# Optimization experiments

Measured on AMD Instinct MI355X. Metric: run time of the kernel, lower is better.

Reference implementation:

```python
import jax, jax.numpy as jnp
import numpy as np
import math

B_SZ, T, D_IN, D_OUT, N = 8, 4096, 1024, 1024, 512
RMIN, RMAX, MAX_PHASE = 0.9, 1.0, 6.283


def setup_inputs() -> dict:
    key = jax.random.key(0)
    ks = jax.random.split(key, 9)
    x = jax.random.normal(ks[0], (B_SZ, T, D_IN), dtype=jnp.float32)
    u1 = jax.random.uniform(ks[1], (N,), dtype=jnp.float32)
    u2 = jax.random.uniform(ks[2], (N,), dtype=jnp.float32)
    nu_log = jnp.log(-0.5 * jnp.log(u1 * (RMAX + RMIN) * (RMAX - RMIN) + RMIN ** 2))
    theta_log = jnp.log(MAX_PHASE * u2)
    lam_mod = jnp.exp(-jnp.exp(nu_log))
    gamma_log = jnp.log(jnp.sqrt(1.0 - jnp.square(lam_mod)))
    B_re = jax.random.normal(ks[3], (N, D_IN), dtype=jnp.float32) / math.sqrt(2 * D_IN)
    B_im = jax.random.normal(ks[4], (N, D_IN), dtype=jnp.float32) / math.sqrt(2 * D_IN)
    C_re = jax.random.normal(ks[5], (D_OUT, N), dtype=jnp.float32) / math.sqrt(N)
    C_im = jax.random.normal(ks[6], (D_OUT, N), dtype=jnp.float32) / math.sqrt(N)
    D = jax.random.normal(ks[7], (D_OUT, D_IN), dtype=jnp.float32) / math.sqrt(D_IN)
    return {"x": x, "nu_log": nu_log, "theta_log": theta_log, "gamma_log": gamma_log,
            "B_re": B_re, "B_im": B_im, "C_re": C_re, "C_im": C_im, "D": D}


def reference(x, nu_log, theta_log, gamma_log, B_re, B_im, C_re, C_im, D):
    # Diagonal complex transition Lambda = exp(-exp(nu_log)) * exp(i*exp(theta_log))
    lam = jnp.exp(-jnp.exp(nu_log) + 1j * jnp.exp(theta_log))  # [N] complex64
    gamma = jnp.exp(gamma_log)  # [N]
    Bmat = B_re + 1j * B_im  # [N, D_IN]
    # Input projection for all timesteps at once: b_t = gamma * (B @ u_t)
    Bu = jnp.einsum('bti,ni->btn', x.astype(Bmat.dtype), Bmat) * gamma  # [B,T,N] complex
    # Parallel (associative) scan of x_t = lam * x_{t-1} + b_t over the time axis
    A = jnp.broadcast_to(lam, Bu.shape)

    def combine(e1, e2):
        a1, b1 = e1
        a2, b2 = e2
        return a1 * a2, a2 * b1 + b2

    _, states = jax.lax.associative_scan(combine, (A, Bu), axis=1)  # states: [B,T,N] complex
    Cmat = C_re + 1j * C_im  # [D_OUT, N]
    y = jnp.einsum('btn,on->bto', states, Cmat).real + jnp.einsum('bti,oi->bto', x, D)
    return y
```

## Files before the change

### kernel.cpp

```cpp
#include <hip/hip_runtime.h>
#include <stdint.h>


#define BSZ   8
#define TLEN  4096
#define DIN   1024
#define DOUT  1024
#define NST   512
#define M_TOT (BSZ * TLEN)
#define NC    32
#define CL    128

#define WOFF  8192
#define NBUF  16384

#define PLA   4096
#define OBUFS 12288

typedef __attribute__((ext_vector_type(8))) short bf16x8;
typedef __attribute__((ext_vector_type(4))) float f32x4;

__device__ __forceinline__ float s2f(short s) {
  unsigned v = ((unsigned)(unsigned short)s) << 16;
  return __builtin_bit_cast(float, v);
}
__device__ __forceinline__ short f2s_rne(float f) {
  unsigned u = __builtin_bit_cast(unsigned, f);
  unsigned r = (u + 0x7FFFu + ((u >> 16) & 1u)) >> 16;
  return (short)r;
}
__device__ __forceinline__ void round8(const float4 v0, const float4 v1, bf16x8& hv) {
  const float f[8] = {v0.x, v0.y, v0.z, v0.w, v1.x, v1.y, v1.z, v1.w};
  #pragma unroll
  for (int j = 0; j < 8; ++j) hv[j] = f2s_rne(f[j]);
}

__device__ __forceinline__ void gload16(const short* g, short* l) {
  __builtin_amdgcn_global_load_lds(
      (const __attribute__((address_space(1))) void*)g,
      (__attribute__((address_space(3))) void*)l, 16, 0, 0);
}


__device__ __forceinline__ void stage_one256(
    const short* __restrict__ Ag, const short* __restrict__ Wg,
    const int lda, const int ldb, const int m0, const int n0, const int k0,
    short* lbuf, const int ch, const int lane)
{
  const int q  = (lane & 3) ^ ((lane >> 3) & 3);
  const int gr = lane >> 2;
  const short* g;
  int r0, ld, dst;
  if (ch < 16) { g = Ag; r0 = m0 + ch * 16;        ld = lda; dst = ch * 512; }
  else         { g = Wg; r0 = n0 + (ch - 16) * 16; ld = ldb; dst = WOFF + (ch - 16) * 512; }
  gload16(g + (size_t)(r0 + gr) * ld + k0 + q * 8, lbuf + dst);
}

template<int NT>
__device__ __forceinline__ void gemm256(
    const short* __restrict__ Ap, const short* __restrict__ Wp,
    const int lda, const int ldb, const int m0, const int n0, const int tid,
    f32x4 (&acc)[8][4], short* lds)
{
  const int lane = tid & 63, w = tid >> 6, wm = w >> 2, wn = w & 3;
  const int lr = lane & 15, kg = lane >> 4;
  const int qo = (kg ^ ((lr >> 1) & 3)) * 8;

  #pragma unroll
  for (int j = 0; j < 4; ++j)
    stage_one256(Ap, Wp, lda, ldb, m0, n0, 0, lds, w * 4 + j, lane);
  #pragma unroll
  for (int j = 0; j < 4; ++j)
    stage_one256(Ap, Wp, lda, ldb, m0, n0, 32, lds + NBUF, w * 4 + j, lane);

  int c0 = 0;
  for (int k = 0; k < NT; ++k) {
    short* cur = lds + c0 * NBUF;
    int cs = c0 + 2; if (cs >= 3) cs -= 3;
    short* nx2 = lds + cs * NBUF;

    if (k + 1 < NT) asm volatile("s_waitcnt vmcnt(4)" ::: "memory");
    else            asm volatile("s_waitcnt vmcnt(0)" ::: "memory");
    __builtin_amdgcn_s_barrier();

    bf16x8 wv[4];
    #pragma unroll
    for (int ph = 0; ph < 4; ++ph) {
      if (ph == 0) {
        #pragma unroll
        for (int nf = 0; nf < 4; ++nf)
          wv[nf] = *(const bf16x8*)&cur[WOFF + (wn * 64 + nf * 16 + lr) * 32 + qo];
      }
      const int mi0 = ph * 2;
      const bf16x8 a0 = *(const bf16x8*)&cur[(wm * 128 + mi0 * 16 + lr) * 32 + qo];
      const bf16x8 a1 = *(const bf16x8*)&cur[(wm * 128 + (mi0 + 1) * 16 + lr) * 32 + qo];
      if (k + 2 < NT)
        stage_one256(Ap, Wp, lda, ldb, m0, n0, (k + 2) * 32, nx2, w * 4 + ph, lane);
      __builtin_amdgcn_s_barrier();
      asm volatile("s_waitcnt lgkmcnt(0)" ::: "memory");
      __builtin_amdgcn_sched_barrier(0);
      __builtin_amdgcn_s_setprio(1);
      #pragma unroll
      for (int nf = 0; nf < 4; ++nf) {
        acc[mi0][nf]     = __builtin_amdgcn_mfma_f32_16x16x32_bf16(a0, wv[nf], acc[mi0][nf], 0, 0, 0);
        acc[mi0 + 1][nf] = __builtin_amdgcn_mfma_f32_16x16x32_bf16(a1, wv[nf], acc[mi0 + 1][nf], 0, 0, 0);
      }
      __builtin_amdgcn_s_setprio(0);
      __builtin_amdgcn_s_barrier();
    }
    c0 = (c0 == 2) ? 0 : c0 + 1;
  }
}

__device__ __forceinline__ void map256(const int bid, int& mb, int& nb) {
  const int xcd = bid & 7;
  const int j   = bid >> 3;
  mb = xcd * 16 + (j >> 2);
  nb = j & 3;
}

__device__ __forceinline__ void stage_cx(
    const short* __restrict__ Ag, const short* __restrict__ Wg,
    const int lda, const int ldb, const int m0, const int n0, const int k0,
    short* lbuf, const int w, const int lane)
{
  const int q  = (lane & 3) ^ ((lane >> 3) & 3);
  const int gr = lane >> 2;
  #pragma unroll
  for (int j = 0; j < 3; ++j) {
    const int ch = w * 3 + j;
    const short* g;
    int r0, ld, dst;
    if (ch < 8) { g = Ag; r0 = m0 + ch * 16;        ld = lda; dst = ch * 512; }
    else        { g = Wg; r0 = n0 + (ch - 8) * 16;  ld = ldb; dst = PLA + (ch - 8) * 512; }
    gload16(g + (size_t)(r0 + gr) * ld + k0 + q * 8, lbuf + dst);
  }
}

__device__ __forceinline__ void gemm_fb(
    const float* __restrict__ Af, const short* __restrict__ Wp,
    const int lda, const int ldb, const int K, const int m0, const int n0, const int tid,
    f32x4 (&acc)[4][4], short* lds)
{
  const int lane = tid & 63, w = tid >> 6, wm = w >> 2, wn = w & 3;
  const int r = tid & 127, e = (tid >> 7) & 3;
  float4 pa[2];
  {
    const float* p = Af + (size_t)(m0 + r) * lda + e * 8;
    pa[0] = *(const float4*)(p);
    pa[1] = *(const float4*)(p + 4);
  }
  for (int k0 = 0; k0 < K; k0 += 32) {
    __syncthreads();
    {
      bf16x8 hv;
      round8(pa[0], pa[1], hv);
      const int f = (r >> 1) & 3;
      *(bf16x8*)&lds[r * 32 + ((e ^ f) * 8)] = hv;
    }
    {
      const int q = (lane & 3) ^ ((lane >> 3) & 3);
      const int gr = lane >> 2;
      #pragma unroll
      for (int i = 0; i < 2; ++i)
        gload16(Wp + (size_t)(n0 + (2 * w + i) * 16 + gr) * ldb + k0 + q * 8,
                lds + PLA + (2 * w + i) * 512);
    }
    __syncthreads();
    if (k0 + 32 < K) {
      const float* p = Af + (size_t)(m0 + r) * lda + (k0 + 32) + e * 8;
      pa[0] = *(const float4*)(p);
      pa[1] = *(const float4*)(p + 4);
    }
    const int lr = lane & 15, kg = lane >> 4;
    const int qo = (kg ^ ((lr >> 1) & 3)) * 8;
    bf16x8 aw[4], bw[4];
    #pragma unroll
    for (int mi = 0; mi < 4; ++mi)
      aw[mi] = *(const bf16x8*)&lds[(wm * 64 + mi * 16 + lr) * 32 + qo];
    #pragma unroll
    for (int ni = 0; ni < 4; ++ni)
      bw[ni] = *(const bf16x8*)&lds[PLA + (wn * 64 + ni * 16 + lr) * 32 + qo];
    #pragma unroll
    for (int ni = 0; ni < 4; ++ni)
      #pragma unroll
      for (int mi = 0; mi < 4; ++mi)
        acc[mi][ni] = __builtin_amdgcn_mfma_f32_16x16x32_bf16(aw[mi], bw[ni], acc[mi][ni], 0, 0, 0);
  }
  __syncthreads();
}

template<int NT>
__device__ __forceinline__ void gemm_pl(
    const short* __restrict__ Ap, const short* __restrict__ Wp,
    const int lda, const int ldb, const int m0, const int n0, const int tid,
    f32x4 (&acc)[4][4], short* lds)
{
  const int lane = tid & 63, w = tid >> 6, wm = w >> 2, wn = w & 3;
  const int lr = lane & 15, kg = lane >> 4;
  const int qo = (kg ^ ((lr >> 1) & 3)) * 8;
  stage_cx(Ap, Wp, lda, ldb, m0, n0, 0, lds, w, lane);
  for (int k = 0; k < NT; ++k) {
    short* cur = lds + (k & 1) * OBUFS;
    if (k + 1 < NT) {
      stage_cx(Ap, Wp, lda, ldb, m0, n0, (k + 1) * 32, lds + ((k + 1) & 1) * OBUFS, w, lane);
      asm volatile("s_waitcnt vmcnt(3)" ::: "memory");
    } else {
      asm volatile("s_waitcnt vmcnt(0)" ::: "memory");
    }
    __builtin_amdgcn_s_barrier();
    bf16x8 bw[4];
    #pragma unroll
    for (int ph = 0; ph < 2; ++ph) {
      if (ph == 0) {
        #pragma unroll
        for (int ni = 0; ni < 4; ++ni)
          bw[ni] = *(const bf16x8*)&cur[PLA + (wn * 64 + ni * 16 + lr) * 32 + qo];
      }
      const int mi0 = ph * 2;
      const bf16x8 a0 = *(const bf16x8*)&cur[(wm * 64 + mi0 * 16 + lr) * 32 + qo];
      const bf16x8 a1 = *(const bf16x8*)&cur[(wm * 64 + (mi0 + 1) * 16 + lr) * 32 + qo];
      __builtin_amdgcn_s_barrier();
      asm volatile("s_waitcnt lgkmcnt(0)" ::: "memory");
      __builtin_amdgcn_sched_barrier(0);
      __builtin_amdgcn_s_setprio(1);
      #pragma unroll
      for (int ni = 0; ni < 4; ++ni) {
        acc[mi0][ni]     = __builtin_amdgcn_mfma_f32_16x16x32_bf16(a0, bw[ni], acc[mi0][ni], 0, 0, 0);
        acc[mi0 + 1][ni] = __builtin_amdgcn_mfma_f32_16x16x32_bf16(a1, bw[ni], acc[mi0 + 1][ni], 0, 0, 0);
      }
      __builtin_amdgcn_s_setprio(0);
      __builtin_amdgcn_s_barrier();
    }
  }
}

__device__ __forceinline__ void map_mn4(const int bid, int& mb, int& nb) {
  const int xcd = bid & 7;
  const int j   = bid >> 3;
  mb = xcd * 32 + (j >> 2);
  nb = j & 3;
}

__global__ __launch_bounds__(256) void wround_k(const float* __restrict__ src,
    short* __restrict__ h, const int n4, const float sgn)
{
  const int i = blockIdx.x * 256 + threadIdx.x;
  if (i >= n4) return;
  const float4 v = ((const float4*)src)[i];
  short4 hv;
  hv.x = f2s_rne(sgn * v.x); hv.y = f2s_rne(sgn * v.y);
  hv.z = f2s_rne(sgn * v.z); hv.w = f2s_rne(sgn * v.w);
  ((short4*)h)[i] = hv;
}

__global__ __launch_bounds__(512, 2) void bu_mfma(
    const short* __restrict__ xw,
    const short* __restrict__ Brw, const short* __restrict__ Biw,
    const float* __restrict__ gamma,
    short* __restrict__ bu_re, short* __restrict__ bu_im)
{
  __shared__ short lds[3 * NBUF];
  f32x4 acc[8][4] = {};
  const int tid = threadIdx.x;
  int mb, nbk;
  map256(blockIdx.x, mb, nbk);
  const int m0  = mb * 256;
  const int n0s = nbk * 256;
  const bool re = (n0s < NST);
  const int nb0 = n0s & (NST - 1);

  gemm256<32>(xw, re ? Brw : Biw, DIN, DIN, m0, nb0, tid, acc, lds);

  short* Hp = re ? bu_re : bu_im;
  const int lane = tid & 63, w = tid >> 6, wm = w >> 2, wn = w & 3;
  const int lr = lane & 15, lq = lane >> 4;
  #pragma unroll
  for (int nf = 0; nf < 4; ++nf) {
    const int nb = nb0 + wn * 64 + nf * 16 + lr;
    const float g = gamma[nb];
    #pragma unroll
    for (int mf = 0; mf < 8; ++mf)
      #pragma unroll
      for (int j = 0; j < 4; ++j) {
        const size_t m = (size_t)m0 + wm * 128 + mf * 16 + lq * 4 + j;
        Hp[m * NST + nb] = f2s_rne(acc[mf][nf][j] * g);
      }
  }
}

__global__ __launch_bounds__(512, 4) void bu_fb(
    const float* __restrict__ x,
    const short* __restrict__ Brw, const short* __restrict__ Biw,
    const float* __restrict__ gamma,
    short* __restrict__ bu_re, short* __restrict__ bu_im)
{
  __shared__ short lds[2 * OBUFS];
  f32x4 acc[4][4] = {};
  const int tid = threadIdx.x;
  int mb, nbk;
  map_mn4(blockIdx.x, mb, nbk);
  const int m0  = mb * 128;
  const int n0s = nbk * 256;
  const bool re = (n0s < NST);
  const int nb0 = n0s & (NST - 1);
  gemm_fb(x, re ? Brw : Biw, DIN, DIN, DIN, m0, nb0, tid, acc, lds);
  short* Hp = re ? bu_re : bu_im;
  const int lane = tid & 63, w = tid >> 6, wm = w >> 2, wn = w & 3;
  const int lr = lane & 15, lq = lane >> 4;
  #pragma unroll
  for (int ni = 0; ni < 4; ++ni) {
    const int nb = nb0 + wn * 64 + ni * 16 + lr;
    const float g = gamma[nb];
    #pragma unroll
    for (int mi = 0; mi < 4; ++mi)
      #pragma unroll
      for (int j = 0; j < 4; ++j) {
        const size_t m = (size_t)m0 + wm * 64 + mi * 16 + lq * 4 + j;
        Hp[m * NST + nb] = f2s_rne(acc[mi][ni][j] * g);
      }
  }
}

__global__ void params_k(const float* __restrict__ nulog, const float* __restrict__ thlog,
                         const float* __restrict__ glog,
                         float2* __restrict__ lam, float2* __restrict__ lamL,
                         float* __restrict__ gamma)
{
  const int n = blockIdx.x * 256 + threadIdx.x;
  if (n >= NST) return;
  const float nu = expf(nulog[n]);
  const float th = expf(thlog[n]);
  const float mod = expf(-nu);
  float s, c;
  sincosf(th, &s, &c);
  lam[n] = make_float2(mod * c, mod * s);
  const float modL = expf(-(float)CL * nu);
  float sL, cL;
  sincosf((float)CL * th, &sL, &cL);
  lamL[n] = make_float2(modL * cL, modL * sL);
  gamma[n] = expf(glog[n]);
}

__global__ __launch_bounds__(256) void scan_partial(
    const short* __restrict__ bu_re, const short* __restrict__ bu_im,
    const float2* __restrict__ lam, float2* __restrict__ carry)
{
  const int g = blockIdx.x * 256 + threadIdx.x;
  const int n2 = g & 255;
  const int c  = (g >> 8) & (NC - 1);
  const int b  = g >> 13;
  const int n  = n2 * 2;
  const float2 L0 = lam[n], L1 = lam[n + 1];
  const short2* R = (const short2*)bu_re;
  const short2* I = (const short2*)bu_im;
  size_t idx = ((size_t)b * TLEN + (size_t)c * CL) * (NST / 2) + n2;
  float sr0 = 0.f, si0 = 0.f, sr1 = 0.f, si1 = 0.f;
  #pragma unroll 4
  for (int t = 0; t < CL; ++t, idx += NST / 2) {
    const short2 vr = R[idx], vi = I[idx];
    const float br0 = s2f(vr.x), br1 = s2f(vr.y);
    const float bi0 = s2f(vi.x), bi1 = s2f(vi.y);
    float nr = fmaf(L0.x, sr0, fmaf(-L0.y, si0, br0));
    float ni = fmaf(L0.x, si0, fmaf( L0.y, sr0, bi0));
    sr0 = nr; si0 = ni;
    nr = fmaf(L1.x, sr1, fmaf(-L1.y, si1, br1));
    ni = fmaf(L1.x, si1, fmaf( L1.y, sr1, bi1));
    sr1 = nr; si1 = ni;
  }
  const size_t cb = (size_t)(b * NC + c) * NST + n;
  carry[cb]     = make_float2(sr0, si0);
  carry[cb + 1] = make_float2(sr1, si1);
}

__global__ __launch_bounds__(256) void scan_carry(
    float2* __restrict__ carry, const float2* __restrict__ lamL)
{
  const int g = blockIdx.x * 256 + threadIdx.x;
  const int n = g & (NST - 1);
  const int b = g >> 9;
  const float2 P = lamL[n];
  float sr = 0.f, si = 0.f;
  for (int c = 0; c < NC; ++c) {
    const size_t idx = (size_t)(b * NC + c) * NST + n;
    const float2 v = carry[idx];
    carry[idx] = make_float2(sr, si);
    const float nr = fmaf(P.x, sr, fmaf(-P.y, si, v.x));
    const float ni = fmaf(P.x, si, fmaf( P.y, sr, v.y));
    sr = nr; si = ni;
  }
}

__global__ __launch_bounds__(256) void scan_final(
    short* __restrict__ bu_re, short* __restrict__ bu_im,
    const float2* __restrict__ lam, const float2* __restrict__ carry)
{
  const int g = blockIdx.x * 256 + threadIdx.x;
  const int n2 = g & 255;
  const int c  = (g >> 8) & (NC - 1);
  const int b  = g >> 13;
  const int n  = n2 * 2;
  const float2 L0 = lam[n], L1 = lam[n + 1];
  const size_t cb = (size_t)(b * NC + c) * NST + n;
  const float2 ci0 = carry[cb], ci1 = carry[cb + 1];
  short2* R = (short2*)bu_re;
  short2* I = (short2*)bu_im;
  size_t idx = ((size_t)b * TLEN + (size_t)c * CL) * (NST / 2) + n2;
  float sr0 = ci0.x, si0 = ci0.y, sr1 = ci1.x, si1 = ci1.y;
  #pragma unroll 4
  for (int t = 0; t < CL; ++t, idx += NST / 2) {
    const short2 vr = R[idx], vi = I[idx];
    const float br0 = s2f(vr.x), br1 = s2f(vr.y);
    const float bi0 = s2f(vi.x), bi1 = s2f(vi.y);
    float nr = fmaf(L0.x, sr0, fmaf(-L0.y, si0, br0));
    float ni = fmaf(L0.x, si0, fmaf( L0.y, sr0, bi0));
    sr0 = nr; si0 = ni;
    nr = fmaf(L1.x, sr1, fmaf(-L1.y, si1, br1));
    ni = fmaf(L1.x, si1, fmaf( L1.y, sr1, bi1));
    sr1 = nr; si1 = ni;
    short2 so;
    so.x = f2s_rne(sr0); so.y = f2s_rne(sr1);
    R[idx] = so;
    so.x = f2s_rne(si0); so.y = f2s_rne(si1);
    I[idx] = so;
  }
}

__global__ __launch_bounds__(512, 2) void out_mfma(
    const short* __restrict__ st_re, const short* __restrict__ st_im,
    const short* __restrict__ xw,
    const short* __restrict__ Crw, const short* __restrict__ Ciw,
    const short* __restrict__ Dw,
    float* __restrict__ y)
{
  __shared__ short lds[3 * NBUF];
  f32x4 acc[8][4] = {};
  const int tid = threadIdx.x;
  int mb, nbk;
  map256(blockIdx.x, mb, nbk);
  const int m0 = mb * 256;
  const int o0 = nbk * 256;

  gemm256<16>(st_re, Crw, NST, NST, m0, o0, tid, acc, lds);
  gemm256<16>(st_im, Ciw, NST, NST, m0, o0, tid, acc, lds);
  gemm256<32>(xw, Dw, DIN, DIN, m0, o0, tid, acc, lds);

  const int lane = tid & 63, w = tid >> 6, wm = w >> 2, wn = w & 3;
  const int lr = lane & 15, lq = lane >> 4;
  #pragma unroll
  for (int mf = 0; mf < 8; ++mf)
    #pragma unroll
    for (int j = 0; j < 4; ++j) {
      const size_t m = (size_t)m0 + wm * 128 + mf * 16 + lq * 4 + j;
      #pragma unroll
      for (int nf = 0; nf < 4; ++nf)
        y[m * DOUT + o0 + wn * 64 + nf * 16 + lr] = acc[mf][nf][j];
    }
}

__global__ __launch_bounds__(512, 4) void out_fb(
    const short* __restrict__ st_re, const short* __restrict__ st_im,
    const float* __restrict__ x,
    const short* __restrict__ Crw, const short* __restrict__ Ciw,
    const short* __restrict__ Dw,
    float* __restrict__ y)
{
  __shared__ short lds[2 * OBUFS];
  f32x4 acc[4][4] = {};
  const int tid = threadIdx.x;
  int mb, nbk;
  map_mn4(blockIdx.x, mb, nbk);
  const int m0 = mb * 128;
  const int o0 = nbk * 256;
  gemm_pl<16>(st_re, Crw, NST, NST, m0, o0, tid, acc, lds);
  gemm_pl<16>(st_im, Ciw, NST, NST, m0, o0, tid, acc, lds);
  gemm_fb(x, Dw, DIN, DIN, DIN, m0, o0, tid, acc, lds);
  const int lane = tid & 63, w = tid >> 6, wm = w >> 2, wn = w & 3;
  const int lr = lane & 15, lq = lane >> 4;
  #pragma unroll
  for (int mi = 0; mi < 4; ++mi)
    #pragma unroll
    for (int j = 0; j < 4; ++j) {
      const size_t m = (size_t)m0 + wm * 64 + mi * 16 + lq * 4 + j;
      #pragma unroll
      for (int ni = 0; ni < 4; ++ni)
        y[m * DOUT + o0 + wn * 64 + ni * 16 + lr] = acc[mi][ni][j];
    }
}

extern "C" void kernel_launch(void* const* d_in, const int* in_sizes, int n_in,
                              void* d_out, int out_size, void* d_ws, size_t ws_size,
                              hipStream_t stream)
{
  (void)in_sizes; (void)n_in; (void)out_size;
  const float* x     = (const float*)d_in[0];
  const float* nulog = (const float*)d_in[1];
  const float* thlog = (const float*)d_in[2];
  const float* glog  = (const float*)d_in[3];
  const float* Bre   = (const float*)d_in[4];
  const float* Bim   = (const float*)d_in[5];
  const float* Cre   = (const float*)d_in[6];
  const float* Cim   = (const float*)d_in[7];
  const float* Dm    = (const float*)d_in[8];
  float* y = (float*)d_out;

  const size_t PLANE  = (size_t)M_TOT * NST;
  const size_t XPLANE = (size_t)M_TOT * DIN;
  short*  bu_re = (short*)d_ws;
  short*  bu_im = bu_re + PLANE;
  float2* carry = (float2*)(bu_im + PLANE);
  float2* lam   = carry + (size_t)BSZ * NC * NST;
  float2* lamL  = lam + NST;
  float*  gamma = (float*)(lamL + NST);

  char* wp = (char*)(gamma + NST);
  wp = (char*)(((uintptr_t)wp + 255) & ~(uintptr_t)255);
  short* Brw = (short*)wp;
  short* Biw = Brw + (size_t)NST * DIN;
  short* Crw = Biw + (size_t)NST * DIN;
  short* Ciw = Crw + (size_t)DOUT * NST;
  short* Dw  = Ciw + (size_t)DOUT * NST;
  short* xw  = Dw  + (size_t)DOUT * DIN;
  const size_t needed_full = (size_t)((char*)(xw + XPLANE) - (char*)d_ws);
  const bool full = (ws_size >= needed_full);

  params_k<<<2, 256, 0, stream>>>(nulog, thlog, glog, lam, lamL, gamma);

  const int nB4 = (NST * DIN) / 4, nC4 = (DOUT * NST) / 4, nD4 = (DOUT * DIN) / 4;
  wround_k<<<(nB4 + 255) / 256, 256, 0, stream>>>(Bre, Brw, nB4,  1.0f);
  wround_k<<<(nB4 + 255) / 256, 256, 0, stream>>>(Bim, Biw, nB4,  1.0f);
  wround_k<<<(nC4 + 255) / 256, 256, 0, stream>>>(Cre, Crw, nC4,  1.0f);
  wround_k<<<(nC4 + 255) / 256, 256, 0, stream>>>(Cim, Ciw, nC4, -1.0f);
  wround_k<<<(nD4 + 255) / 256, 256, 0, stream>>>(Dm,  Dw,  nD4,  1.0f);

  if (full) {
    const int nX4 = (int)(XPLANE / 4);
    wround_k<<<(nX4 + 255) / 256, 256, 0, stream>>>(x, xw, nX4, 1.0f);
    bu_mfma<<<512, 512, 0, stream>>>(xw, Brw, Biw, gamma, bu_re, bu_im);
  } else {
    bu_fb<<<1024, 512, 0, stream>>>(x, Brw, Biw, gamma, bu_re, bu_im);
  }

  scan_partial<<<(BSZ * NC * (NST / 2)) / 256, 256, 0, stream>>>(bu_re, bu_im, lam, carry);
  scan_carry<<<(BSZ * NST) / 256, 256, 0, stream>>>(carry, lamL);
  scan_final<<<(BSZ * NC * (NST / 2)) / 256, 256, 0, stream>>>(bu_re, bu_im, lam, carry);

  if (full) {
    out_mfma<<<512, 512, 0, stream>>>(bu_re, bu_im, xw, Crw, Ciw, Dw, y);
  } else {
    out_fb<<<1024, 512, 0, stream>>>(bu_re, bu_im, x, Crw, Ciw, Dw, y);
  }
}
```

Measured before the change: 307.5 us.

## Use K=64 double-buffered GEMM pipeline and fuse bf16 rounding launches

The shared GEMM routine switches from a three-stage, K=32-per-step ring buffer to a double-buffered scheme in which each iteration processes two K=32 sub-tiles (K=64), with the whole next tile prefetched at the top of the loop. Iteration counts are halved to match. This halves the number of barrier-separated iterations and should amortise synchronisation per MFMA, but prefetch now issues in one burst instead of being spread across the phases, and LDS use rises from 96KB to 128KB per block. Separately, six weight/input bf16 rounding launches are merged into one kernel to cut launch overhead.

```diff
diff --git a/kernel.cpp b/kernel.cpp
--- a/kernel.cpp
+++ b/kernel.cpp
@@ -12,7 +12,8 @@
 #define CL    128
 
 #define WOFF  8192
-#define NBUF  16384
+#define SUB   16384
+#define TBUF  32768
 
 #define PLA   4096
 #define OBUFS 12288
@@ -67,48 +68,58 @@
   const int qo = (kg ^ ((lr >> 1) & 3)) * 8;
 
   #pragma unroll
-  for (int j = 0; j < 4; ++j)
-    stage_one256(Ap, Wp, lda, ldb, m0, n0, 0, lds, w * 4 + j, lane);
-  #pragma unroll
-  for (int j = 0; j < 4; ++j)
-    stage_one256(Ap, Wp, lda, ldb, m0, n0, 32, lds + NBUF, w * 4 + j, lane);
-
-  int c0 = 0;
+  for (int s = 0; s < 2; ++s)
+    #pragma unroll
+    for (int j = 0; j < 4; ++j)
+      stage_one256(Ap, Wp, lda, ldb, m0, n0, s * 32, lds + s * SUB, w * 4 + j, lane);
+
   for (int k = 0; k < NT; ++k) {
-    short* cur = lds + c0 * NBUF;
-    int cs = c0 + 2; if (cs >= 3) cs -= 3;
-    short* nx2 = lds + cs * NBUF;
-
-    if (k + 1 < NT) asm volatile("s_waitcnt vmcnt(4)" ::: "memory");
-    else            asm volatile("s_waitcnt vmcnt(0)" ::: "memory");
+    short* cur = lds + (k & 1) * TBUF;
+    if (k + 1 < NT) {
+      short* nxt = lds + ((k + 1) & 1) * TBUF;
+      #pragma unroll
+      for (int s = 0; s < 2; ++s)
+        #pragma unroll
+        for (int j = 0; j < 4; ++j)
+          stage_one256(Ap, Wp, lda, ldb, m0, n0, (k + 1) * 64 + s * 32,
+                       nxt + s * SUB, w * 4 + j, lane);
+      asm volatile("s_waitcnt vmcnt(8)" ::: "memory");
+    } else {
+      asm volatile("s_waitcnt vmcnt(0)" ::: "memory");
+    }
     __builtin_amdgcn_s_barrier();
 
-    bf16x8 wv[4];
+    bf16x8 wv[2][4];
     #pragma unroll
     for (int ph = 0; ph < 4; ++ph) {
       if (ph == 0) {
         #pragma unroll
-        for (int nf = 0; nf < 4; ++nf)
-          wv[nf] = *(const bf16x8*)&cur[WOFF + (wn * 64 + nf * 16 + lr) * 32 + qo];
+        for (int s = 0; s < 2; ++s)
+          #pragma unroll
+          for (int nf = 0; nf < 4; ++nf)
+            wv[s][nf] = *(const bf16x8*)&cur[s * SUB + WOFF + (wn * 64 + nf * 16 + lr) * 32 + qo];
       }
       const int mi0 = ph * 2;
-      const bf16x8 a0 = *(const bf16x8*)&cur[(wm * 128 + mi0 * 16 + lr) * 32 + qo];
-      const bf16x8 a1 = *(const bf16x8*)&cur[(wm * 128 + (mi0 + 1) * 16 + lr) * 32 + qo];
-      if (k + 2 < NT)
-        stage_one256(Ap, Wp, lda, ldb, m0, n0, (k + 2) * 32, nx2, w * 4 + ph, lane);
+      bf16x8 a[2][2];
+      #pragma unroll
+      for (int s = 0; s < 2; ++s) {
+        a[s][0] = *(const bf16x8*)&cur[s * SUB + (wm * 128 + mi0 * 16 + lr) * 32 + qo];
+        a[s][1] = *(const bf16x8*)&cur[s * SUB + (wm * 128 + (mi0 + 1) * 16 + lr) * 32 + qo];
+      }
       __builtin_amdgcn_s_barrier();
       asm volatile("s_waitcnt lgkmcnt(0)" ::: "memory");
       __builtin_amdgcn_sched_barrier(0);
       __builtin_amdgcn_s_setprio(1);
       #pragma unroll
-      for (int nf = 0; nf < 4; ++nf) {
-        acc[mi0][nf]     = __builtin_amdgcn_mfma_f32_16x16x32_bf16(a0, wv[nf], acc[mi0][nf], 0, 0, 0);
-        acc[mi0 + 1][nf] = __builtin_amdgcn_mfma_f32_16x16x32_bf16(a1, wv[nf], acc[mi0 + 1][nf], 0, 0, 0);
-      }
+      for (int s = 0; s < 2; ++s)
+        #pragma unroll
+        for (int nf = 0; nf < 4; ++nf) {
+          acc[mi0][nf]     = __builtin_amdgcn_mfma_f32_16x16x32_bf16(a[s][0], wv[s][nf], acc[mi0][nf], 0, 0, 0);
+          acc[mi0 + 1][nf] = __builtin_amdgcn_mfma_f32_16x16x32_bf16(a[s][1], wv[s][nf], acc[mi0 + 1][nf], 0, 0, 0);
+        }
       __builtin_amdgcn_s_setprio(0);
       __builtin_amdgcn_s_barrier();
     }
-    c0 = (c0 == 2) ? 0 : c0 + 1;
   }
 }
 
@@ -242,16 +253,29 @@
   nb = j & 3;
 }
 
-__global__ __launch_bounds__(256) void wround_k(const float* __restrict__ src,
-    short* __restrict__ h, const int n4, const float sgn)
-{
-  const int i = blockIdx.x * 256 + threadIdx.x;
-  if (i >= n4) return;
-  const float4 v = ((const float4*)src)[i];
+__global__ __launch_bounds__(256) void wround_all(
+    const float* __restrict__ Bre, const float* __restrict__ Bim,
+    const float* __restrict__ Cre, const float* __restrict__ Cim,
+    const float* __restrict__ Dm,  const float* __restrict__ x,
+    short* __restrict__ Brw, short* __restrict__ Biw,
+    short* __restrict__ Crw, short* __restrict__ Ciw,
+    short* __restrict__ Dw,  short* __restrict__ xw,
+    const int nB4, const int nC4, const int nD4, const int nX4)
+{
+  int o = blockIdx.x * 256 + threadIdx.x;
+  const float* src; short* dst; float sgn = 1.0f;
+  if (o < nB4)              { src = Bre; dst = Brw; }
+  else if ((o -= nB4) < nB4){ src = Bim; dst = Biw; }
+  else if ((o -= nB4) < nC4){ src = Cre; dst = Crw; }
+  else if ((o -= nC4) < nC4){ src = Cim; dst = Ciw; sgn = -1.0f; }
+  else if ((o -= nC4) < nD4){ src = Dm;  dst = Dw; }
+  else if ((o -= nD4) < nX4){ src = x;   dst = xw; }
+  else return;
+  const float4 v = ((const float4*)src)[o];
   short4 hv;
   hv.x = f2s_rne(sgn * v.x); hv.y = f2s_rne(sgn * v.y);
   hv.z = f2s_rne(sgn * v.z); hv.w = f2s_rne(sgn * v.w);
-  ((short4*)h)[i] = hv;
+  ((short4*)dst)[o] = hv;
 }
 
 __global__ __launch_bounds__(512, 2) void bu_mfma(
@@ -260,7 +284,7 @@
     const float* __restrict__ gamma,
     short* __restrict__ bu_re, short* __restrict__ bu_im)
 {
-  __shared__ short lds[3 * NBUF];
+  __shared__ short lds[2 * TBUF];
   f32x4 acc[8][4] = {};
   const int tid = threadIdx.x;
   int mb, nbk;
@@ -270,7 +294,7 @@
   const bool re = (n0s < NST);
   const int nb0 = n0s & (NST - 1);
 
-  gemm256<32>(xw, re ? Brw : Biw, DIN, DIN, m0, nb0, tid, acc, lds);
+  gemm256<16>(xw, re ? Brw : Biw, DIN, DIN, m0, nb0, tid, acc, lds);
 
   short* Hp = re ? bu_re : bu_im;
   const int lane = tid & 63, w = tid >> 6, wm = w >> 2, wn = w & 3;
@@ -433,7 +457,7 @@
     const short* __restrict__ Dw,
     float* __restrict__ y)
 {
-  __shared__ short lds[3 * NBUF];
+  __shared__ short lds[2 * TBUF];
   f32x4 acc[8][4] = {};
   const int tid = threadIdx.x;
   int mb, nbk;
@@ -441,9 +465,9 @@
   const int m0 = mb * 256;
   const int o0 = nbk * 256;
 
-  gemm256<16>(st_re, Crw, NST, NST, m0, o0, tid, acc, lds);
-  gemm256<16>(st_im, Ciw, NST, NST, m0, o0, tid, acc, lds);
-  gemm256<32>(xw, Dw, DIN, DIN, m0, o0, tid, acc, lds);
+  gemm256<8>(st_re, Crw, NST, NST, m0, o0, tid, acc, lds);
+  gemm256<8>(st_im, Ciw, NST, NST, m0, o0, tid, acc, lds);
+  gemm256<16>(xw, Dw, DIN, DIN, m0, o0, tid, acc, lds);
 
   const int lane = tid & 63, w = tid >> 6, wm = w >> 2, wn = w & 3;
   const int lr = lane & 15, lq = lane >> 4;
@@ -527,15 +551,12 @@
   params_k<<<2, 256, 0, stream>>>(nulog, thlog, glog, lam, lamL, gamma);
 
   const int nB4 = (NST * DIN) / 4, nC4 = (DOUT * NST) / 4, nD4 = (DOUT * DIN) / 4;
-  wround_k<<<(nB4 + 255) / 256, 256, 0, stream>>>(Bre, Brw, nB4,  1.0f);
-  wround_k<<<(nB4 + 255) / 256, 256, 0, stream>>>(Bim, Biw, nB4,  1.0f);
-  wround_k<<<(nC4 + 255) / 256, 256, 0, stream>>>(Cre, Crw, nC4,  1.0f);
-  wround_k<<<(nC4 + 255) / 256, 256, 0, stream>>>(Cim, Ciw, nC4, -1.0f);
-  wround_k<<<(nD4 + 255) / 256, 256, 0, stream>>>(Dm,  Dw,  nD4,  1.0f);
+  const int nX4 = full ? (int)(XPLANE / 4) : 0;
+  const int tot4 = 2 * nB4 + 2 * nC4 + nD4 + nX4;
+  wround_all<<<(tot4 + 255) / 256, 256, 0, stream>>>(
+      Bre, Bim, Cre, Cim, Dm, x, Brw, Biw, Crw, Ciw, Dw, xw, nB4, nC4, nD4, nX4);
 
   if (full) {
-    const int nX4 = (int)(XPLANE / 4);
-    wround_k<<<(nX4 + 255) / 256, 256, 0, stream>>>(x, xw, nX4, 1.0f);
     bu_mfma<<<512, 512, 0, stream>>>(xw, Brw, Biw, gamma, bu_re, bu_im);
   } else {
     bu_fb<<<1024, 512, 0, stream>>>(x, Brw, Biw, gamma, bu_re, bu_im);
```

Measured after the change: 326.4 us. 6.2% more time.
